# Kernel tuning notes

Hardware: AMD Instinct MI355X
Metric: run time of the kernel (lower is better)

The kernel has to match this reference:

```python
import jax, jax.numpy as jnp
import numpy as np
from jax import lax
from jax.scipy.special import digamma, logsumexp

EPS = 1e-9
T, K, D = 20000, 64, 32
Kp1 = K + 1


def setup_inputs():
    key = jax.random.key(0)
    ks = jax.random.split(key, 8)
    z_mu = jax.random.normal(ks[0], (T, D), dtype=jnp.float32)
    z_var = jax.random.uniform(ks[1], (T, D), minval=0.05, maxval=1.0, dtype=jnp.float32)
    mu_hat = jax.random.normal(ks[2], (Kp1, D), dtype=jnp.float32)
    kappa_hat = 0.01 + 100.0 * jax.random.uniform(ks[3], (Kp1,), dtype=jnp.float32)
    # nu_hat must exceed D+1; emulate nu0 + Nk with nu0 = max(32, D+2) = 34
    nu_hat = 34.0 + 100.0 * jax.random.uniform(ks[4], (Kp1,), dtype=jnp.float32)
    A = 0.1 * jax.random.normal(ks[5], (Kp1, D, D), dtype=jnp.float32)
    Psi_hat = jnp.eye(D, dtype=jnp.float32)[None] + jnp.einsum('kij,klj->kil', A, A)  # SPD
    phi_hat = 0.1 + 5.0 * jax.random.uniform(ks[6], (K, Kp1), dtype=jnp.float32)
    w = jax.random.uniform(ks[7], (Kp1,), minval=0.1, maxval=1.0, dtype=jnp.float32)
    pi_star = w / w.sum()
    return dict(z_mu=z_mu, z_var=z_var, mu_hat=mu_hat, kappa_hat=kappa_hat,
                nu_hat=nu_hat, Psi_hat=Psi_hat, phi_hat=phi_hat, pi_star=pi_star)


def reference(z_mu, z_var, mu_hat, kappa_hat, nu_hat, Psi_hat, phi_hat, pi_star):
    LOG2PI = float(np.log(2.0 * np.pi))
    LOG2 = float(np.log(2.0))
    # ---- expected emission log-likelihood E_q[log N(z_t | mu_k, Sigma_k)] : (T, K+1) ----
    d_arange = jnp.arange(1, D + 1, dtype=jnp.float32)
    E_logdet = (digamma((nu_hat[:, None] + 1.0 - d_arange) * 0.5).sum(-1)
                - D * LOG2 - jnp.linalg.slogdet(Psi_hat)[1])  # (Kp1,)
    Lam = nu_hat[:, None, None] * jnp.linalg.inv(Psi_hat)      # E[Lambda_k] (Kp1,D,D)
    t1 = jnp.einsum('kd,td->tk', jnp.diagonal(Lam, axis1=-2, axis2=-1), z_var)
    diff = z_mu[:, None, :] - mu_hat[None, :, :]               # (T,Kp1,D)
    t2 = jnp.einsum('tki,kij,tkj->tk', diff, Lam, diff)
    t3 = D * nu_hat / (kappa_hat * jnp.clip(nu_hat - D - 1.0, 1.0))
    log_B = -0.5 * (E_logdet[None, :] + t1 + t2 + t3[None, :] + D * LOG2PI)

    # ---- expected log transition matrix / initial dist ----
    log_A = digamma(phi_hat) - digamma(phi_hat.sum(-1, keepdims=True))  # (K,Kp1)
    log_pi = jnp.log(pi_star + EPS)                                      # (Kp1,)

    # ---- forward recursion (lax.scan over T) ----
    def fwd_step(prev, logb):
        msg = logsumexp(prev[:K, None] + log_A, axis=0)
        msg = jnp.logaddexp(msg, prev[-1] + log_pi)
        new = logb + msg
        return new, new
    a0 = log_pi + log_B[0]
    _, alphas = lax.scan(fwd_step, a0, log_B[1:])
    log_alpha = jnp.concatenate([a0[None], alphas], axis=0)  # (T,Kp1)

    # ---- backward recursion (reverse scan) ----
    def bwd_step(nxt, logb_next):
        tmp = logb_next + nxt  # (Kp1,)
        bk = logsumexp(log_A + tmp[None, :], axis=1)  # (K,)
        blast = logsumexp(log_pi + tmp)
        new = jnp.concatenate([bk, blast[None]])
        return new, new
    bT = jnp.zeros((Kp1,), dtype=log_B.dtype)
    _, betas = lax.scan(bwd_step, bT, log_B[1:], reverse=True)
    log_beta = jnp.concatenate([betas, bT[None]], axis=0)  # (T,Kp1)

    logZ = logsumexp(log_alpha[-1])
    gamma = jax.nn.softmax(log_alpha + log_beta - logZ, axis=-1)

    # ---- pairwise posteriors xi : (T-1, K, Kp1), vectorized over t ----
    bb = log_B[1:] + log_beta[1:]  # (T-1,Kp1)
    temp = jnp.logaddexp(log_alpha[:-1, :K, None] + log_A[None] + bb[:, None, :],
                         (log_pi + bb)[:, None, :])
    norm = logsumexp(temp.reshape(T - 1, K * Kp1), axis=-1)
    xi = jnp.exp(temp - norm[:, None, None])
    return gamma, xi, logZ
```

## Files before the change

kernel.cpp:

```cpp
#include <hip/hip_runtime.h>
#include <math.h>

#define T_LEN 20000
#define KST 64
#define KP1 65
#define DD 32
#define CHK 250
#define LCH 80

static __device__ __forceinline__ float wsum64(float v){
  v += __shfl_xor(v, 1);  v += __shfl_xor(v, 2);  v += __shfl_xor(v, 4);
  v += __shfl_xor(v, 8);  v += __shfl_xor(v, 16); v += __shfl_xor(v, 32);
  return v;
}
static __device__ __forceinline__ float wmax64(float v){
  v = fmaxf(v, __shfl_xor(v, 1));  v = fmaxf(v, __shfl_xor(v, 2));  v = fmaxf(v, __shfl_xor(v, 4));
  v = fmaxf(v, __shfl_xor(v, 8));  v = fmaxf(v, __shfl_xor(v, 16)); v = fmaxf(v, __shfl_xor(v, 32));
  return v;
}
static __device__ __forceinline__ float readlane_f(float v, int i){
  return __int_as_float(__builtin_amdgcn_readlane(__float_as_int(v), i));
}
static __device__ __forceinline__ float digamma_f(float x){
  float r = 0.f;
  while (x < 6.f){ r -= 1.f / x; x += 1.f; }
  float xi = 1.f / x;
  float xi2 = xi * xi;
  return r + logf(x) - 0.5f * xi
       - xi2 * (0.08333333333f - xi2 * (0.008333333333f - xi2 * 0.003968253968f));
}
static __device__ __forceinline__ float rcp_nr(float s){
  float r = __builtin_amdgcn_rcpf(s);
  return r * (2.0f - s * r);
}

__global__ void prep_k(const float* __restrict__ mu, const float* __restrict__ kappa,
                       const float* __restrict__ nu, const float* __restrict__ Psi,
                       float* __restrict__ Lam, float* __restrict__ dLam,
                       float* __restrict__ constk){
  const int k = blockIdx.x, tid = threadIdx.x;
  __shared__ float P[DD][DD + 1];
  const float* Pk = Psi + k * DD * DD;
  for (int e = tid; e < DD * DD; e += 64) P[e / DD][e % DD] = Pk[e];
  __syncthreads();
  for (int c = 0; c < DD; ++c){
    if (tid == c){
      float s = P[c][c];
      for (int m = 0; m < c; ++m) s -= P[c][m] * P[c][m];
      P[c][c] = sqrtf(s);
    }
    __syncthreads();
    if (tid > c && tid < DD){
      float s = P[tid][c];
      for (int m = 0; m < c; ++m) s -= P[tid][m] * P[c][m];
      P[tid][c] = s / P[c][c];
    }
    __syncthreads();
  }
  const float nuk = nu[k];
  if (tid < DD){
    float y[DD];
    #pragma unroll
    for (int r2 = 0; r2 < DD; ++r2){
      float s = (r2 == tid) ? 1.f : 0.f;
      #pragma unroll
      for (int m = 0; m < r2; ++m) s -= P[r2][m] * y[m];
      y[r2] = s / P[r2][r2];
    }
    #pragma unroll
    for (int r2 = DD - 1; r2 >= 0; --r2){
      float s = y[r2];
      #pragma unroll
      for (int m = r2 + 1; m < DD; ++m) s -= P[m][r2] * y[m];
      y[r2] = s / P[r2][r2];
    }
    #pragma unroll
    for (int i = 0; i < DD; ++i) Lam[k * DD * DD + i * DD + tid] = nuk * y[i];
    dLam[k * DD + tid] = nuk * y[tid];
  }
  float dg = 0.f, ld = 0.f;
  if (tid < DD){
    dg = digamma_f((nuk + 1.f - (float)(tid + 1)) * 0.5f);
    ld = logf(P[tid][tid]);
  }
  dg = wsum64(dg);
  ld = wsum64(ld);
  if (tid == 0){
    const float LOG2 = 0.6931471805599453f, LOG2PI = 1.8378770664093453f;
    float logdet = 2.f * ld;
    float Elogdet = dg - DD * LOG2 - logdet;
    float t3 = DD * nuk / (kappa[k] * fmaxf(nuk - DD - 1.f, 1.f));
    constk[k] = -0.5f * (Elogdet + t3 + DD * LOG2PI);
  }
}

__global__ void prep_trans(const float* __restrict__ phi, const float* __restrict__ pi_star,
                           float* __restrict__ M_mat, float* __restrict__ MT,
                           float* __restrict__ logA, float* __restrict__ logpi){
  const int i = threadIdx.x;
  float rs = 0.f;
  for (int j = 0; j < KP1; ++j) rs += phi[i * KP1 + j];
  float dgs = digamma_f(rs);
  for (int j = 0; j < KP1; ++j){
    float la = digamma_f(phi[i * KP1 + j]) - dgs;
    logA[i * KP1 + j] = la;
    float e = expf(la);
    M_mat[i * 68 + j] = e;
    MT[j * 68 + i] = e;
  }
  if (i == 0){
    for (int j = 0; j < KP1; ++j){
      float pe = pi_star[j] + 1e-9f;
      logpi[j] = logf(pe);
      M_mat[64 * 68 + j] = pe;
      MT[j * 68 + 64] = pe;
    }
  }
}

__global__ void logb_k(const float* __restrict__ zmu, const float* __restrict__ zvar,
                       const float* __restrict__ mu, const float* __restrict__ Lam,
                       const float* __restrict__ dLam, const float* __restrict__ constk,
                       float* __restrict__ logB){
  const int k = blockIdx.y, tid = threadIdx.x;
  const int t = blockIdx.x * 256 + tid;
  __shared__ float Ls[DD * DD];
  __shared__ float mus[DD], dls[DD];
  for (int e = tid; e < DD * DD; e += 256) Ls[e] = Lam[k * DD * DD + e];
  if (tid < DD){ mus[tid] = mu[k * DD + tid]; dls[tid] = dLam[k * DD + tid]; }
  __syncthreads();
  if (t >= T_LEN) return;
  const float4* zm4 = reinterpret_cast<const float4*>(zmu + (size_t)t * DD);
  const float4* zv4 = reinterpret_cast<const float4*>(zvar + (size_t)t * DD);
  float d[DD];
  float acc1 = 0.f;
  #pragma unroll
  for (int q = 0; q < DD / 4; ++q){
    float4 vm = zm4[q]; float4 vv = zv4[q];
    d[4*q+0] = vm.x - mus[4*q+0];
    d[4*q+1] = vm.y - mus[4*q+1];
    d[4*q+2] = vm.z - mus[4*q+2];
    d[4*q+3] = vm.w - mus[4*q+3];
    acc1 = fmaf(dls[4*q+0], vv.x, acc1);
    acc1 = fmaf(dls[4*q+1], vv.y, acc1);
    acc1 = fmaf(dls[4*q+2], vv.z, acc1);
    acc1 = fmaf(dls[4*q+3], vv.w, acc1);
  }
  float acc2 = 0.f;
  #pragma unroll
  for (int i = 0; i < DD; ++i){
    float s = 0.f;
    #pragma unroll
    for (int q = 0; q < DD/4; ++q){
      float4 L4 = *reinterpret_cast<const float4*>(&Ls[i*DD + q*4]);
      s = fmaf(L4.x, d[q*4+0], s);
      s = fmaf(L4.y, d[q*4+1], s);
      s = fmaf(L4.z, d[q*4+2], s);
      s = fmaf(L4.w, d[q*4+3], s);
    }
    acc2 = fmaf(s, d[i], acc2);
  }
  logB[(size_t)t * KP1 + k] = constk[k] - 0.5f * (acc1 + acc2);
}

__global__ void bexp_k(const float* __restrict__ logB, float* __restrict__ Bexp,
                       float* __restrict__ bmax){
  const int lane = threadIdx.x & 63, w = threadIdx.x >> 6;
  const int t = blockIdx.x * 4 + w;
  if (t >= T_LEN) return;
  float v = logB[(size_t)t * KP1 + lane];
  float v64 = logB[(size_t)t * KP1 + 64];
  float m = fmaxf(wmax64(v), v64);
  Bexp[(size_t)t * KP1 + lane] = expf(v - m);
  if (lane == 0){ Bexp[(size_t)t * KP1 + 64] = expf(v64 - m); bmax[t] = m; }
}

__global__ __launch_bounds__(64) void p1_k(const float* __restrict__ MT_g,
    const float* __restrict__ Bexp, float* __restrict__ S){
  __shared__ float MTl[65 * 68];
  __shared__ float Xl[64 * 65];
  const int lane = threadIdx.x;
  const int dir = blockIdx.y;
  for (int e = lane; e < 65 * 68; e += 64) MTl[e] = MT_g[e];
  __syncthreads();
  const int bx = blockIdx.x;
  const bool service = bx >= CHK;
  const int c = service ? bx - CHK : bx;
  int r0, r1;
  if (dir == 0){ r0 = 1 + c * LCH; r1 = min((c + 1) * LCH, T_LEN - 1); }
  else {
    int ue = min((c + 1) * LCH, T_LEN - 1) - 1;
    r0 = (T_LEN - 1) - ue; r1 = (T_LEN - 1) - c * LCH;
  }
  float* Sc = S + (size_t)(dir * CHK + c) * 4290;
  float* sig_out = Sc + 4225;

  if (!service){
    #pragma unroll
    for (int k = 0; k < 65; ++k) Xl[lane * 65 + k] = (k == lane) ? 1.f : 0.f;
    float rs = 1.f, sig = 0.f;
    float bvec = Bexp[(size_t)r0 * KP1 + lane];
    float b64  = Bexp[(size_t)r0 * KP1 + 64];
    for (int r = r0; r <= r1; ++r){
      float bvn = 0.f, b64n = 0.f;
      if (r < r1){
        bvn  = Bexp[(size_t)(r + 1) * KP1 + lane];
        b64n = Bexp[(size_t)(r + 1) * KP1 + 64];
      }
      float Xr[65];
      #pragma unroll
      for (int k = 0; k < 65; ++k) Xr[k] = Xl[lane * 65 + k] * rs;
      #pragma unroll
      for (int k = 0; k < 65; ++k) Xl[lane * 65 + k] = 0.f;
      unsigned long long mask = __ballot(bvec != 0.f);
      float cmax = 0.f;
      while (mask){
        int i = __builtin_ctzll(mask); mask &= mask - 1;
        float bi = readlane_f(bvec, i);
        const float* Mr = &MTl[i * 68];
        float a0 = 0.f, a1 = 0.f, a2 = 0.f, a3 = 0.f;
        #pragma unroll
        for (int g = 0; g < 16; ++g){
          float4 m4 = *reinterpret_cast<const float4*>(&Mr[g * 4]);
          a0 = fmaf(m4.x, Xr[g * 4 + 0], a0);
          a1 = fmaf(m4.y, Xr[g * 4 + 1], a1);
          a2 = fmaf(m4.z, Xr[g * 4 + 2], a2);
          a3 = fmaf(m4.w, Xr[g * 4 + 3], a3);
        }
        float sum = ((a0 + a1) + (a2 + a3)) + Mr[64] * Xr[64];
        float nv = bi * sum;
        Xl[lane * 65 + i] = nv;
        cmax = fmaxf(cmax, nv);
      }
      if (b64 != 0.f){
        const float* Mr = &MTl[64 * 68];
        float a0 = 0.f, a1 = 0.f, a2 = 0.f, a3 = 0.f;
        #pragma unroll
        for (int g = 0; g < 16; ++g){
          float4 m4 = *reinterpret_cast<const float4*>(&Mr[g * 4]);
          a0 = fmaf(m4.x, Xr[g * 4 + 0], a0);
          a1 = fmaf(m4.y, Xr[g * 4 + 1], a1);
          a2 = fmaf(m4.z, Xr[g * 4 + 2], a2);
          a3 = fmaf(m4.w, Xr[g * 4 + 3], a3);
        }
        float sum = ((a0 + a1) + (a2 + a3)) + Mr[64] * Xr[64];
        float nv = b64 * sum;
        Xl[lane * 65 + 64] = nv;
        cmax = fmaxf(cmax, nv);
      }
      float s = wmax64(cmax);
      s = fmaxf(s, 1e-37f);
      sig += logf(s);
      rs = 1.f / s;
      bvec = bvn; b64 = b64n;
    }
    for (int k = 0; k < 65; ++k) Sc[k * 65 + lane] = Xl[lane * 65 + k] * rs;
    sig_out[lane] = sig;
  } else {
    float v = 0.f, v64 = 1.f, sig = 0.f;
    float bvec = Bexp[(size_t)r0 * KP1 + lane];
    float b64  = Bexp[(size_t)r0 * KP1 + 64];
    for (int r = r0; r <= r1; ++r){
      float bvn = 0.f, b64n = 0.f;
      if (r < r1){
        bvn  = Bexp[(size_t)(r + 1) * KP1 + lane];
        b64n = Bexp[(size_t)(r + 1) * KP1 + 64];
      }
      unsigned long long mask = __ballot(bvec != 0.f);
      float vn = 0.f, v64n = 0.f;
      while (mask){
        int i = __builtin_ctzll(mask); mask &= mask - 1;
        float mi = MTl[i * 68 + lane];
        float t = mi * v;
        float sum = wsum64(t) + MTl[i * 68 + 64] * v64;
        float bi = readlane_f(bvec, i);
        vn = (lane == i) ? bi * sum : vn;
      }
      if (b64 != 0.f){
        float t = MTl[64 * 68 + lane] * v;
        float sum = wsum64(t) + MTl[64 * 68 + 64] * v64;
        v64n = b64 * sum;
      }
      float m = wmax64(vn);
      m = fmaxf(m, v64n);
      m = fmaxf(m, 1e-37f);
      float irs = 1.f / m;
      v = vn * irs; v64 = v64n * irs;
      sig += logf(m);
      bvec = bvn; b64 = b64n;
    }
    Sc[lane * 65 + 64] = v;
    if (lane == 0){ Sc[64 * 65 + 64] = v64; sig_out[64] = sig; }
  }
}

__global__ __launch_bounds__(256) void p2_k(const float* __restrict__ S,
    const float* __restrict__ M_mat, const float* __restrict__ Bexp,
    float* __restrict__ vstore){
  const int dir = blockIdx.x, tid = threadIdx.x;
  __shared__ float Sl[4290];
  __shared__ float vl[66];
  __shared__ float red[1];
  if (dir == 0){
    if (tid < 65) vl[tid] = M_mat[64 * 68 + tid] * Bexp[tid];
  } else {
    if (tid < 65) vl[tid] = 1.f;
  }
  __syncthreads();
  if (tid < 64){
    float x = vl[tid];
    float s = wsum64(x) + vl[64];
    if (tid == 0) red[0] = 1.f / s;
  }
  __syncthreads();
  if (tid < 65) vl[tid] *= red[0];
  const float* Sg = S + (size_t)dir * CHK * 4290;
  float sb[17];
  #pragma unroll
  for (int u = 0; u < 17; ++u){
    int e = tid + 256 * u;
    sb[u] = (e < 4290) ? Sg[e] : 0.f;
  }
  for (int c = 0; c < CHK; ++c){
    __syncthreads();
    #pragma unroll
    for (int u = 0; u < 17; ++u){
      int e = tid + 256 * u;
      if (e < 4290) Sl[e] = sb[u];
    }
    __syncthreads();
    if (c + 1 < CHK){
      const float* Sn = Sg + (size_t)(c + 1) * 4290;
      #pragma unroll
      for (int u = 0; u < 17; ++u){
        int e = tid + 256 * u;
        sb[u] = (e < 4290) ? Sn[e] : 0.f;
      }
    }
    if (tid < 65){
      vstore[(size_t)(dir * CHK + c) * KP1 + tid] = vl[tid];
      float sm = fmaxf(Sl[4225], Sl[4225 + 64]);
      vl[tid] = vl[tid] * expf(Sl[4225 + tid] - sm);
    }
    __syncthreads();
    float vn = 0.f;
    if (tid < 65){
      if (dir == 0){
        for (int j = 0; j < 65; ++j) vn = fmaf(Sl[tid * 65 + j], vl[j], vn);
      } else {
        for (int k = 0; k < 65; ++k) vn = fmaf(Sl[k * 65 + tid], vl[k], vn);
      }
    }
    __syncthreads();
    if (tid < 65) vl[tid] = vn;
    __syncthreads();
    if (tid < 64){
      float x = vl[tid];
      float s = wsum64(x) + vl[64];
      if (tid == 0) red[0] = 1.f / fmaxf(s, 1e-37f);
    }
    __syncthreads();
    if (tid < 65) vl[tid] *= red[0];
  }
}

__global__ __launch_bounds__(64) void p3_k(const float* __restrict__ M_mat,
    const float* __restrict__ MT_g, const float* __restrict__ Bexp,
    const float* __restrict__ bmax, const float* __restrict__ vstore,
    float* __restrict__ pstore, float* __restrict__ qstore,
    float* __restrict__ cfor, float* __restrict__ csum){
  __shared__ float Ml[65 * 68];
  const int lane = threadIdx.x;
  const int c = blockIdx.x, dir = blockIdx.y;
  const float* src = (dir == 0) ? M_mat : MT_g;
  for (int e = lane; e < 65 * 68; e += 64) Ml[e] = src[e];
  __syncthreads();
  if (dir == 0){
    float p, p64, sig;
    const int r0 = 1 + c * LCH, r1 = min((c + 1) * LCH, T_LEN - 1);
    if (c == 0){
      float pe = Ml[64 * 68 + lane], pe64 = Ml[64 * 68 + 64];
      float b = Bexp[lane], b64v = Bexp[64];
      float val = pe * b, v64 = pe64 * b64v;
      float s = wsum64(val) + v64;
      float rr = 1.f / s;
      p = val * rr; p64 = v64 * rr;
      pstore[lane] = p; if (lane == 0) pstore[64] = p64;
      sig = logf(s) + bmax[0];
      if (lane == 0) cfor[0] = sig;
    } else {
      p = vstore[(size_t)c * KP1 + lane];
      p64 = vstore[(size_t)c * KP1 + 64];
      sig = 0.f;
    }
    float bvec = Bexp[(size_t)r0 * KP1 + lane], b64 = Bexp[(size_t)r0 * KP1 + 64];
    for (int r = r0; r <= r1; ++r){
      float bvn = 0.f, b64n = 0.f;
      if (r < r1){
        bvn = Bexp[(size_t)(r + 1) * KP1 + lane]; b64n = Bexp[(size_t)(r + 1) * KP1 + 64];
      }
      unsigned long long mask = __ballot(p != 0.f);
      float msg = 0.f, msg64 = 0.f;
      while (mask){
        int i = __builtin_ctzll(mask); mask &= mask - 1;
        float pi_ = readlane_f(p, i);
        msg   = fmaf(pi_, Ml[i * 68 + lane], msg);
        msg64 = fmaf(pi_, Ml[i * 68 + 64], msg64);
      }
      if (p64 != 0.f){
        msg   = fmaf(p64, Ml[64 * 68 + lane], msg);
        msg64 = fmaf(p64, Ml[64 * 68 + 64], msg64);
      }
      float val = bvec * msg, v64 = b64 * msg64;
      float s = wsum64(val) + v64;
      float rr = 1.f / s;
      p = val * rr; p64 = v64 * rr;
      pstore[(size_t)r * KP1 + lane] = p;
      if (lane == 0) pstore[(size_t)r * KP1 + 64] = p64;
      sig += logf(s) + bmax[r];
      if (lane == 0) cfor[r] = sig;
      bvec = bvn; b64 = b64n;
    }
    if (lane == 0) csum[c] = sig;
  } else {
    float q, q64;
    const int ustart = c * LCH;
    const int ue = min((c + 1) * LCH, T_LEN - 1) - 1;
    if (c == 0){
      q = 1.f / 65.f; q64 = 1.f / 65.f;
      qstore[(size_t)(T_LEN - 1) * KP1 + lane] = q;
      if (lane == 0) qstore[(size_t)(T_LEN - 1) * KP1 + 64] = q64;
    } else {
      q = vstore[(size_t)(CHK + c) * KP1 + lane];
      q64 = vstore[(size_t)(CHK + c) * KP1 + 64];
    }
    int rfirst = (T_LEN - 1) - ustart;
    float bvec = Bexp[(size_t)rfirst * KP1 + lane], b64 = Bexp[(size_t)rfirst * KP1 + 64];
    for (int u = ustart; u <= ue; ++u){
      int r = (T_LEN - 1) - u;
      float bvn = 0.f, b64n = 0.f;
      if (u < ue){
        bvn = Bexp[(size_t)(r - 1) * KP1 + lane]; b64n = Bexp[(size_t)(r - 1) * KP1 + 64];
      }
      float x = bvec * q, x64 = b64 * q64;
      unsigned long long mask = __ballot(x != 0.f);
      float acc = 0.f, acc64 = 0.f;
      while (mask){
        int k = __builtin_ctzll(mask); mask &= mask - 1;
        float xk = readlane_f(x, k);
        acc   = fmaf(xk, Ml[k * 68 + lane], acc);
        acc64 = fmaf(xk, Ml[k * 68 + 64], acc64);
      }
      if (x64 != 0.f){
        acc   = fmaf(x64, Ml[64 * 68 + lane], acc);
        acc64 = fmaf(x64, Ml[64 * 68 + 64], acc64);
      }
      float s = wsum64(acc) + acc64;
      float rr = 1.f / s;
      q = acc * rr; q64 = acc64 * rr;
      qstore[(size_t)(r - 1) * KP1 + lane] = q;
      if (lane == 0) qstore[(size_t)(r - 1) * KP1 + 64] = q64;
      bvec = bvn; b64 = b64n;
    }
  }
}

__global__ __launch_bounds__(64) void pfx_k(const float* __restrict__ csum,
    float* __restrict__ coff, float* __restrict__ logZ){
  __shared__ float cs[CHK], co[CHK + 1];
  const int lane = threadIdx.x;
  for (int e = lane; e < CHK; e += 64) cs[e] = csum[e];
  __syncthreads();
  if (lane == 0){
    float a = 0.f;
    for (int c = 0; c < CHK; ++c){ co[c] = a; a += cs[c]; }
    co[CHK] = a;
    logZ[0] = a;
  }
  __syncthreads();
  for (int e = lane; e < CHK; e += 64) coff[e] = co[e];
}

__global__ void off_k(float* __restrict__ cfor, const float* __restrict__ coff){
  int t = blockIdx.x * 256 + threadIdx.x;
  if (t >= T_LEN) return;
  int c = (t == 0) ? 0 : (t - 1) / LCH;
  cfor[t] += coff[c];
}

__global__ void gamma_k(const float* __restrict__ pstore, const float* __restrict__ qstore,
                        float* __restrict__ gout){
  const int lane = threadIdx.x & 63, w = threadIdx.x >> 6;
  const int t = blockIdx.x * 4 + w;
  if (t >= T_LEN) return;
  float a   = pstore[(size_t)t * KP1 + lane] * qstore[(size_t)t * KP1 + lane];
  float a64 = pstore[(size_t)t * KP1 + 64]   * qstore[(size_t)t * KP1 + 64];
  float s = wsum64(a) + a64;
  float r = rcp_nr(s);
  gout[(size_t)t * KP1 + lane] = a * r;
  if (lane == 0) gout[(size_t)t * KP1 + 64] = a64 * r;
}

__global__ void xi_k(const float* __restrict__ pstore, const float* __restrict__ qstore,
                     const float* __restrict__ logB, const float* __restrict__ cfor,
                     const float* __restrict__ logA, const float* __restrict__ logpi,
                     float* __restrict__ xiout){
  const int t = blockIdx.x, tid = threadIdx.x;
  __shared__ float laS[64], bbS[KP1], lpiS[KP1];
  __shared__ float red[4], red2[4];
  if (tid < 64){
    laS[tid] = logf(pstore[(size_t)t * KP1 + tid]) + cfor[t];
  } else if (tid < 64 + KP1){
    int j = tid - 64;
    bbS[j] = logB[(size_t)(t + 1) * KP1 + j] + logf(qstore[(size_t)(t + 1) * KP1 + j]);
  } else if (tid < 64 + 2 * KP1){
    int j = tid - (64 + KP1);
    lpiS[j] = logpi[j];
  }
  __syncthreads();
  float tv[17];
  float lm = -3.0e38f;
  #pragma unroll
  for (int r2 = 0; r2 < 17; ++r2){
    int e = tid + 256 * r2;
    if (e < KST * KP1){
      int i = e / KP1;
      int j = e - i * KP1;
      float a = laS[i] + logA[e];
      float b = lpiS[j];
      float mx = fmaxf(a, b), mn = fminf(a, b);
      float v = bbS[j] + mx + log1pf(expf(mn - mx));
      tv[r2] = v;
      lm = fmaxf(lm, v);
    } else tv[r2] = -3.0e38f;
  }
  lm = wmax64(lm);
  if ((tid & 63) == 0) red[tid >> 6] = lm;
  __syncthreads();
  float gm = fmaxf(fmaxf(red[0], red[1]), fmaxf(red[2], red[3]));
  float se = 0.f;
  #pragma unroll
  for (int r2 = 0; r2 < 17; ++r2) se += expf(tv[r2] - gm);
  se = wsum64(se);
  if ((tid & 63) == 0) red2[tid >> 6] = se;
  __syncthreads();
  float S = red2[0] + red2[1] + red2[2] + red2[3];
  float rS = rcp_nr(S);
  float* xrow = xiout + (size_t)t * (KST * KP1);
  #pragma unroll
  for (int r2 = 0; r2 < 17; ++r2){
    int e = tid + 256 * r2;
    if (e < KST * KP1) xrow[e] = expf(tv[r2] - gm) * rS;
  }
}

extern "C" void kernel_launch(void* const* d_in, const int* in_sizes, int n_in,
                              void* d_out, int out_size, void* d_ws, size_t ws_size,
                              hipStream_t stream){
  const float* z_mu  = (const float*)d_in[0];
  const float* z_var = (const float*)d_in[1];
  const float* mu    = (const float*)d_in[2];
  const float* kappa = (const float*)d_in[3];
  const float* nu    = (const float*)d_in[4];
  const float* Psi   = (const float*)d_in[5];
  const float* phi   = (const float*)d_in[6];
  const float* pis   = (const float*)d_in[7];
  float* out = (float*)d_out;

  float* ws     = (float*)d_ws;
  float* Lam    = ws;
  float* dLam   = Lam + 66560;
  float* constk = dLam + 2080;
  float* M_mat  = constk + 65;
  float* MT     = M_mat + 4420;
  float* logA   = MT + 4420;
  float* logpi  = logA + 4160;
  float* logB   = logpi + 65;
  float* Bexp   = logB + 1300000;
  float* bmax   = Bexp + 1300000;
  float* pstore = bmax + 20000;
  float* qstore = pstore + 1300000;
  float* cfor   = qstore + 1300000;
  float* S      = cfor + 20000;
  float* vstore = S + 2145000;
  float* csum   = vstore + 32500;
  float* coff   = csum + 256;

  float* gammaOut = out;
  float* xiOut    = gammaOut + (size_t)T_LEN * KP1;
  float* logZOut  = xiOut + (size_t)(T_LEN - 1) * KST * KP1;

  prep_k<<<KP1, 64, 0, stream>>>(mu, kappa, nu, Psi, Lam, dLam, constk);
  prep_trans<<<1, 64, 0, stream>>>(phi, pis, M_mat, MT, logA, logpi);
  logb_k<<<dim3((T_LEN + 255) / 256, KP1), 256, 0, stream>>>(z_mu, z_var, mu, Lam, dLam, constk, logB);
  bexp_k<<<(T_LEN + 3) / 4, 256, 0, stream>>>(logB, Bexp, bmax);
  p1_k<<<dim3(2 * CHK, 2), 64, 0, stream>>>(MT, Bexp, S);
  p2_k<<<2, 256, 0, stream>>>(S, M_mat, Bexp, vstore);
  p3_k<<<dim3(CHK, 2), 64, 0, stream>>>(M_mat, MT, Bexp, bmax, vstore, pstore, qstore, cfor, csum);
  pfx_k<<<1, 64, 0, stream>>>(csum, coff, logZOut);
  off_k<<<(T_LEN + 255) / 256, 256, 0, stream>>>(cfor, coff);
  gamma_k<<<(T_LEN + 3) / 4, 256, 0, stream>>>(pstore, qstore, gammaOut);
  xi_k<<<T_LEN - 1, 256, 0, stream>>>(pstore, qstore, logB, cfor, logA, logpi, xiOut);
}
```

Measured before the change: 1.365 ms.

## Add hierarchical chunk-operator scan, sparse transfer products, and xi smem/logaddexp tweaks

```diff
diff --git a/kernel.cpp b/kernel.cpp
--- a/kernel.cpp
+++ b/kernel.cpp
@@ -7,6 +7,9 @@
 #define DD 32
 #define CHK 250
 #define LCH 80
+#define GSZ 10
+#define NG 25
+#define OPS 4296
 
 static __device__ __forceinline__ float wsum64(float v){
   v += __shfl_xor(v, 1);  v += __shfl_xor(v, 2);  v += __shfl_xor(v, 4);
@@ -178,7 +181,7 @@
 __global__ __launch_bounds__(64) void p1_k(const float* __restrict__ MT_g,
     const float* __restrict__ Bexp, float* __restrict__ S){
   __shared__ float MTl[65 * 68];
-  __shared__ float Xl[64 * 65];
+  __shared__ float Xbuf[2][65][64];
   const int lane = threadIdx.x;
   const int dir = blockIdx.y;
   for (int e = lane; e < 65 * 68; e += 64) MTl[e] = MT_g[e];
@@ -192,70 +195,103 @@
     int ue = min((c + 1) * LCH, T_LEN - 1) - 1;
     r0 = (T_LEN - 1) - ue; r1 = (T_LEN - 1) - c * LCH;
   }
-  float* Sc = S + (size_t)(dir * CHK + c) * 4290;
+  float* Sc = S + (size_t)(dir * CHK + c) * OPS;
   float* sig_out = Sc + 4225;
 
   if (!service){
-    #pragma unroll
-    for (int k = 0; k < 65; ++k) Xl[lane * 65 + k] = (k == lane) ? 1.f : 0.f;
     float rs = 1.f, sig = 0.f;
-    float bvec = Bexp[(size_t)r0 * KP1 + lane];
-    float b64  = Bexp[(size_t)r0 * KP1 + 64];
+    unsigned long long pmask = 0; bool pb64 = false;
+    unsigned long long dirty0 = ~0ull, dirty1 = ~0ull;
+    bool dirty64_0 = true, dirty64_1 = true;
+    int cur = 0;
+    float bv0 = Bexp[(size_t)r0 * KP1 + lane];
+    float b640 = Bexp[(size_t)r0 * KP1 + 64];
+    float bv1 = 0.f, b641 = 0.f;
+    if (r0 + 1 <= r1){ bv1 = Bexp[(size_t)(r0+1) * KP1 + lane]; b641 = Bexp[(size_t)(r0+1) * KP1 + 64]; }
     for (int r = r0; r <= r1; ++r){
-      float bvn = 0.f, b64n = 0.f;
-      if (r < r1){
-        bvn  = Bexp[(size_t)(r + 1) * KP1 + lane];
-        b64n = Bexp[(size_t)(r + 1) * KP1 + 64];
-      }
-      float Xr[65];
-      #pragma unroll
-      for (int k = 0; k < 65; ++k) Xr[k] = Xl[lane * 65 + k] * rs;
-      #pragma unroll
-      for (int k = 0; k < 65; ++k) Xl[lane * 65 + k] = 0.f;
-      unsigned long long mask = __ballot(bvec != 0.f);
+      float bv2 = 0.f, b642 = 0.f;
+      if (r + 2 <= r1){ bv2 = Bexp[(size_t)(r+2) * KP1 + lane]; b642 = Bexp[(size_t)(r+2) * KP1 + 64]; }
+      unsigned long long nmask = __ballot(bv0 != 0.f);
+      bool nb64 = (b640 != 0.f);
+      const int nb = cur ^ 1;
       float cmax = 0.f;
-      while (mask){
-        int i = __builtin_ctzll(mask); mask &= mask - 1;
-        float bi = readlane_f(bvec, i);
-        const float* Mr = &MTl[i * 68];
-        float a0 = 0.f, a1 = 0.f, a2 = 0.f, a3 = 0.f;
-        #pragma unroll
-        for (int g = 0; g < 16; ++g){
-          float4 m4 = *reinterpret_cast<const float4*>(&Mr[g * 4]);
-          a0 = fmaf(m4.x, Xr[g * 4 + 0], a0);
-          a1 = fmaf(m4.y, Xr[g * 4 + 1], a1);
-          a2 = fmaf(m4.z, Xr[g * 4 + 2], a2);
-          a3 = fmaf(m4.w, Xr[g * 4 + 3], a3);
+      if (r == r0){
+        unsigned long long m = nmask;
+        while (m){
+          int i = __builtin_ctzll(m); m &= m - 1;
+          float nv = readlane_f(bv0, i) * MTl[i*68 + lane];
+          Xbuf[nb][i][lane] = nv; cmax = fmaxf(cmax, nv);
         }
-        float sum = ((a0 + a1) + (a2 + a3)) + Mr[64] * Xr[64];
-        float nv = bi * sum;
-        Xl[lane * 65 + i] = nv;
-        cmax = fmaxf(cmax, nv);
-      }
-      if (b64 != 0.f){
-        const float* Mr = &MTl[64 * 68];
-        float a0 = 0.f, a1 = 0.f, a2 = 0.f, a3 = 0.f;
-        #pragma unroll
-        for (int g = 0; g < 16; ++g){
-          float4 m4 = *reinterpret_cast<const float4*>(&Mr[g * 4]);
-          a0 = fmaf(m4.x, Xr[g * 4 + 0], a0);
-          a1 = fmaf(m4.y, Xr[g * 4 + 1], a1);
-          a2 = fmaf(m4.z, Xr[g * 4 + 2], a2);
-          a3 = fmaf(m4.w, Xr[g * 4 + 3], a3);
+        if (nb64){
+          float nv = b640 * MTl[64*68 + lane];
+          Xbuf[nb][64][lane] = nv; cmax = fmaxf(cmax, nv);
         }
-        float sum = ((a0 + a1) + (a2 + a3)) + Mr[64] * Xr[64];
-        float nv = b64 * sum;
-        Xl[lane * 65 + 64] = nv;
-        cmax = fmaxf(cmax, nv);
-      }
-      float s = wmax64(cmax);
-      s = fmaxf(s, 1e-37f);
+      } else {
+        const bool dense = __builtin_popcountll(pmask) >= 24;
+        for (int pass = 0; pass < 2; ++pass){
+          if (pass == 1 && !nb64) break;
+          unsigned long long mm = (pass == 0) ? nmask : 1ull;
+          while (mm){
+            int i;
+            if (pass == 0){ i = __builtin_ctzll(mm); mm &= mm - 1; }
+            else { i = 64; mm = 0; }
+            float acc = 0.f;
+            if (dense){
+              #pragma unroll
+              for (int g4 = 0; g4 < 16; ++g4){
+                float4 m4 = *reinterpret_cast<const float4*>(&MTl[i*68 + 4*g4]);
+                acc = fmaf(m4.x, Xbuf[cur][4*g4+0][lane], acc);
+                acc = fmaf(m4.y, Xbuf[cur][4*g4+1][lane], acc);
+                acc = fmaf(m4.z, Xbuf[cur][4*g4+2][lane], acc);
+                acc = fmaf(m4.w, Xbuf[cur][4*g4+3][lane], acc);
+              }
+              acc = fmaf(MTl[i*68 + 64], Xbuf[cur][64][lane], acc);
+            } else {
+              unsigned long long jm = pmask;
+              while (jm){
+                int j = __builtin_ctzll(jm); jm &= jm - 1;
+                acc = fmaf(MTl[i*68 + j], Xbuf[cur][j][lane], acc);
+              }
+              if (pb64) acc = fmaf(MTl[i*68 + 64], Xbuf[cur][64][lane], acc);
+            }
+            float bi = (i == 64) ? b640 : readlane_f(bv0, i);
+            float nv = bi * acc * rs;
+            Xbuf[nb][i][lane] = nv;
+            cmax = fmaxf(cmax, nv);
+          }
+        }
+      }
+      {
+        unsigned long long dN = (nb == 0) ? dirty0 : dirty1;
+        bool d64N = (nb == 0) ? dirty64_0 : dirty64_1;
+        unsigned long long zm = dN & ~nmask;
+        while (zm){
+          int z = __builtin_ctzll(zm); zm &= zm - 1;
+          Xbuf[nb][z][lane] = 0.f;
+        }
+        if (d64N && !nb64) Xbuf[nb][64][lane] = 0.f;
+        if (nb == 0){ dirty0 = nmask; dirty64_0 = nb64; }
+        else        { dirty1 = nmask; dirty64_1 = nb64; }
+      }
+      float s = fmaxf(wmax64(cmax), 1e-37f);
       sig += logf(s);
       rs = 1.f / s;
-      bvec = bvn; b64 = b64n;
-    }
-    for (int k = 0; k < 65; ++k) Sc[k * 65 + lane] = Xl[lane * 65 + k] * rs;
+      pmask = nmask; pb64 = nb64;
+      cur = nb;
+      bv0 = bv1; b640 = b641; bv1 = bv2; b641 = b642;
+    }
+    for (int i = 0; i < 65; ++i){
+      bool act = (i < 64) ? ((pmask >> i) & 1ull) : pb64;
+      float v = act ? Xbuf[cur][i][lane] * rs : 0.f;
+      Sc[i * 65 + lane] = v;
+    }
     sig_out[lane] = sig;
+    if (lane == 0){
+      unsigned int* mw = (unsigned int*)Sc;
+      mw[4290] = (unsigned int)(pmask & 0xffffffffull);
+      mw[4291] = (unsigned int)(pmask >> 32);
+      mw[4292] = pb64 ? 1u : 0u;
+    }
   } else {
     float v = 0.f, v64 = 1.f, sig = 0.f;
     float bvec = Bexp[(size_t)r0 * KP1 + lane];
@@ -294,61 +330,210 @@
   }
 }
 
-__global__ __launch_bounds__(256) void p2_k(const float* __restrict__ S,
+__global__ __launch_bounds__(256) void p2a_k(const float* __restrict__ S,
+    float* __restrict__ Gop){
+  const int tid = threadIdx.x, lane = tid & 63, wv = tid >> 6;
+  const int g = blockIdx.x, dir = blockIdx.y;
+  __shared__ float Ys[65 * 65];
+  __shared__ float Gt[65 * 65];
+  __shared__ float Scl[OPS];
+  __shared__ float ysig[65];
+  __shared__ unsigned int msh[3];
+  const float* base = S + (size_t)(dir * CHK + g * GSZ) * OPS;
+  if (dir == 0){
+    for (int e = tid; e < 4225; e += 256) Ys[e] = base[e];
+  } else {
+    for (int e = tid; e < 4225; e += 256){
+      int i = e / 65, j = e - i * 65;
+      Ys[j * 65 + i] = base[e];
+    }
+  }
+  if (tid < 65) ysig[tid] = base[4225 + tid];
+  if (tid < 3) msh[tid] = ((const unsigned int*)base)[4290 + tid];
+  __syncthreads();
+  for (int cc = 1; cc < GSZ; ++cc){
+    const float* opc = base + (size_t)cc * OPS;
+    for (int e = tid; e < OPS; e += 256) Scl[e] = opc[e];
+    __syncthreads();
+    if (wv == 0){
+      float sigm = Scl[4225 + 0];
+      float sigs = Scl[4225 + 64];
+      float smc = fmaxf(sigm, sigs);
+      float rfm = expf(sigm - smc), rfs = expf(sigs - smc);
+      if (dir == 0){
+        unsigned long long pm = (unsigned long long)msh[0] | ((unsigned long long)msh[1] << 32);
+        bool pb64 = (msh[2] & 1u) != 0;
+        const unsigned int* smw = (const unsigned int*)Scl;
+        unsigned long long im = (unsigned long long)smw[4290] | ((unsigned long long)smw[4291] << 32);
+        bool ib64 = (smw[4292] & 1u) != 0;
+        const bool dense = __builtin_popcountll(pm) >= 24;
+        float colmax = 0.f, col64max = 0.f;
+        for (int i = 0; i < 65; ++i){
+          bool act = (i < 64) ? ((im >> i) & 1ull) : ib64;
+          float acc = 0.f, acc64 = 0.f;
+          if (act){
+            if (dense){
+              for (int k = 0; k < 64; ++k)
+                acc = fmaf(Scl[i*65 + k], Ys[k*65 + lane], acc);
+              acc *= rfm;
+            } else {
+              unsigned long long jm = pm;
+              while (jm){
+                int k = __builtin_ctzll(jm); jm &= jm - 1;
+                acc = fmaf(Scl[i*65 + k], Ys[k*65 + lane], acc);
+              }
+              acc *= rfm;
+            }
+            if (pb64) acc = fmaf(rfs * Scl[i*65 + 64], Ys[64*65 + lane], acc);
+            float part = rfm * Scl[i*65 + lane] * Ys[lane*65 + 64];
+            acc64 = wsum64(part);
+            if (pb64) acc64 += rfs * Scl[i*65 + 64] * Ys[64*65 + 64];
+          }
+          Gt[i*65 + lane] = acc;
+          if (lane == 0) Gt[i*65 + 64] = acc64;
+          colmax = fmaxf(colmax, acc);
+          col64max = fmaxf(col64max, acc64);
+        }
+        float mj = fmaxf(colmax, 1e-37f);
+        float inv = 1.f / mj;
+        for (int i = 0; i < 65; ++i) Ys[i*65 + lane] = Gt[i*65 + lane] * inv;
+        ysig[lane] += logf(mj) + smc;
+        if (lane == 0){
+          float m64 = fmaxf(col64max, 1e-37f);
+          float i64 = 1.f / m64;
+          for (int i = 0; i < 65; ++i) Ys[i*65 + 64] = Gt[i*65 + 64] * i64;
+          ysig[64] += logf(m64) + smc;
+          msh[0] = (unsigned int)(im & 0xffffffffull);
+          msh[1] = (unsigned int)(im >> 32);
+          msh[2] = ib64 ? 1u : 0u;
+        }
+      } else {
+        float colmax = 0.f, col64max = 0.f;
+        for (int i = 0; i < 65; ++i){
+          float acc = 0.f;
+          for (int k = 0; k < 64; ++k)
+            acc = fmaf(Scl[k*65 + i], Ys[k*65 + lane], acc);
+          acc *= rfm;
+          acc = fmaf(rfs * Scl[64*65 + i], Ys[64*65 + lane], acc);
+          float part = rfm * Scl[lane*65 + i] * Ys[lane*65 + 64];
+          float acc64 = wsum64(part) + rfs * Scl[64*65 + i] * Ys[64*65 + 64];
+          Gt[i*65 + lane] = acc;
+          if (lane == 0) Gt[i*65 + 64] = acc64;
+          colmax = fmaxf(colmax, acc);
+          col64max = fmaxf(col64max, acc64);
+        }
+        float mj = fmaxf(colmax, 1e-37f);
+        float inv = 1.f / mj;
+        for (int i = 0; i < 65; ++i) Ys[i*65 + lane] = Gt[i*65 + lane] * inv;
+        ysig[lane] += logf(mj) + smc;
+        if (lane == 0){
+          float m64 = fmaxf(col64max, 1e-37f);
+          float i64 = 1.f / m64;
+          for (int i = 0; i < 65; ++i) Ys[i*65 + 64] = Gt[i*65 + 64] * i64;
+          ysig[64] += logf(m64) + smc;
+        }
+      }
+    }
+    __syncthreads();
+  }
+  float* outp = Gop + (size_t)(dir * NG + g) * OPS;
+  for (int e = tid; e < 4225; e += 256) outp[e] = Ys[e];
+  if (tid < 65) outp[4225 + tid] = ysig[tid];
+  if (tid < 3) ((unsigned int*)outp)[4290 + tid] = msh[tid];
+}
+
+__global__ __launch_bounds__(256) void p2b_k(const float* __restrict__ Gop,
     const float* __restrict__ M_mat, const float* __restrict__ Bexp,
-    float* __restrict__ vstore){
+    float* __restrict__ gseed){
   const int dir = blockIdx.x, tid = threadIdx.x;
-  __shared__ float Sl[4290];
+  __shared__ float Sl[OPS];
   __shared__ float vl[66];
-  __shared__ float red[1];
-  if (dir == 0){
-    if (tid < 65) vl[tid] = M_mat[64 * 68 + tid] * Bexp[tid];
-  } else {
-    if (tid < 65) vl[tid] = 1.f;
-  }
+  __shared__ float red[2];
+  if (dir == 0){ if (tid < 65) vl[tid] = M_mat[64*68 + tid] * Bexp[tid]; }
+  else { if (tid < 65) vl[tid] = 1.f; }
   __syncthreads();
   if (tid < 64){
     float x = vl[tid];
     float s = wsum64(x) + vl[64];
-    if (tid == 0) red[0] = 1.f / s;
+    if (tid == 0) red[0] = 1.f / fmaxf(s, 1e-37f);
   }
   __syncthreads();
   if (tid < 65) vl[tid] *= red[0];
-  const float* Sg = S + (size_t)dir * CHK * 4290;
+  const float* Gg = Gop + (size_t)dir * NG * OPS;
   float sb[17];
   #pragma unroll
-  for (int u = 0; u < 17; ++u){
-    int e = tid + 256 * u;
-    sb[u] = (e < 4290) ? Sg[e] : 0.f;
-  }
-  for (int c = 0; c < CHK; ++c){
+  for (int u = 0; u < 17; ++u){ int e = tid + 256*u; sb[u] = (e < OPS) ? Gg[e] : 0.f; }
+  for (int c = 0; c < NG; ++c){
     __syncthreads();
     #pragma unroll
-    for (int u = 0; u < 17; ++u){
-      int e = tid + 256 * u;
-      if (e < 4290) Sl[e] = sb[u];
-    }
-    __syncthreads();
-    if (c + 1 < CHK){
-      const float* Sn = Sg + (size_t)(c + 1) * 4290;
+    for (int u = 0; u < 17; ++u){ int e = tid + 256*u; if (e < OPS) Sl[e] = sb[u]; }
+    __syncthreads();
+    if (c + 1 < NG){
+      const float* Sn = Gg + (size_t)(c+1) * OPS;
       #pragma unroll
-      for (int u = 0; u < 17; ++u){
-        int e = tid + 256 * u;
-        sb[u] = (e < 4290) ? Sn[e] : 0.f;
-      }
-    }
+      for (int u = 0; u < 17; ++u){ int e = tid + 256*u; sb[u] = (e < OPS) ? Sn[e] : 0.f; }
+    }
+    if (tid < 65) gseed[(size_t)(dir * NG + c) * KP1 + tid] = vl[tid];
+    if (tid < 64){
+      float gm = wmax64(Sl[4225 + tid]);
+      if (tid == 0) red[1] = fmaxf(gm, Sl[4225 + 64]);
+    }
+    __syncthreads();
+    if (tid < 65) vl[tid] = vl[tid] * expf(Sl[4225 + tid] - red[1]);
+    __syncthreads();
+    float vn = 0.f;
     if (tid < 65){
-      vstore[(size_t)(dir * CHK + c) * KP1 + tid] = vl[tid];
-      float sm = fmaxf(Sl[4225], Sl[4225 + 64]);
-      vl[tid] = vl[tid] * expf(Sl[4225 + tid] - sm);
-    }
+      for (int j = 0; j < 65; ++j) vn = fmaf(Sl[tid*65 + j], vl[j], vn);
+    }
+    __syncthreads();
+    if (tid < 65) vl[tid] = vn;
+    __syncthreads();
+    if (tid < 64){
+      float x = vl[tid];
+      float s = wsum64(x) + vl[64];
+      if (tid == 0) red[0] = 1.f / fmaxf(s, 1e-37f);
+    }
+    __syncthreads();
+    if (tid < 65) vl[tid] *= red[0];
+  }
+}
+
+__global__ __launch_bounds__(256) void p2c_k(const float* __restrict__ S,
+    const float* __restrict__ gseed, float* __restrict__ vstore){
+  const int g = blockIdx.x, dir = blockIdx.y, tid = threadIdx.x;
+  __shared__ float Sl[OPS];
+  __shared__ float vl[66];
+  __shared__ float red[2];
+  if (tid < 65) vl[tid] = gseed[(size_t)(dir * NG + g) * KP1 + tid];
+  const float* base = S + (size_t)(dir * CHK + g * GSZ) * OPS;
+  float sb[17];
+  #pragma unroll
+  for (int u = 0; u < 17; ++u){ int e = tid + 256*u; sb[u] = (e < OPS) ? base[e] : 0.f; }
+  for (int cc = 0; cc < GSZ; ++cc){
+    __syncthreads();
+    #pragma unroll
+    for (int u = 0; u < 17; ++u){ int e = tid + 256*u; if (e < OPS) Sl[e] = sb[u]; }
+    __syncthreads();
+    if (cc + 1 < GSZ){
+      const float* Sn = base + (size_t)(cc+1) * OPS;
+      #pragma unroll
+      for (int u = 0; u < 17; ++u){ int e = tid + 256*u; sb[u] = (e < OPS) ? Sn[e] : 0.f; }
+    }
+    const int cid = g * GSZ + cc;
+    if (tid < 65) vstore[(size_t)(dir * CHK + cid) * KP1 + tid] = vl[tid];
+    if (tid < 64){
+      float gm = wmax64(Sl[4225 + tid]);
+      if (tid == 0) red[1] = fmaxf(gm, Sl[4225 + 64]);
+    }
+    __syncthreads();
+    if (tid < 65) vl[tid] = vl[tid] * expf(Sl[4225 + tid] - red[1]);
     __syncthreads();
     float vn = 0.f;
     if (tid < 65){
       if (dir == 0){
-        for (int j = 0; j < 65; ++j) vn = fmaf(Sl[tid * 65 + j], vl[j], vn);
+        for (int j = 0; j < 65; ++j) vn = fmaf(Sl[tid*65 + j], vl[j], vn);
       } else {
-        for (int k = 0; k < 65; ++k) vn = fmaf(Sl[k * 65 + tid], vl[k], vn);
+        for (int k = 0; k < 65; ++k) vn = fmaf(Sl[k*65 + tid], vl[k], vn);
       }
     }
     __syncthreads();
@@ -383,10 +568,10 @@
       float b = Bexp[lane], b64v = Bexp[64];
       float val = pe * b, v64 = pe64 * b64v;
       float s = wsum64(val) + v64;
-      float rr = 1.f / s;
+      float rr = 1.f / fmaxf(s, 1e-37f);
       p = val * rr; p64 = v64 * rr;
       pstore[lane] = p; if (lane == 0) pstore[64] = p64;
-      sig = logf(s) + bmax[0];
+      sig = logf(fmaxf(s, 1e-37f)) + bmax[0];
       if (lane == 0) cfor[0] = sig;
     } else {
       p = vstore[(size_t)c * KP1 + lane];
@@ -413,11 +598,11 @@
       }
       float val = bvec * msg, v64 = b64 * msg64;
       float s = wsum64(val) + v64;
-      float rr = 1.f / s;
+      float rr = 1.f / fmaxf(s, 1e-37f);
       p = val * rr; p64 = v64 * rr;
       pstore[(size_t)r * KP1 + lane] = p;
       if (lane == 0) pstore[(size_t)r * KP1 + 64] = p64;
-      sig += logf(s) + bmax[r];
+      sig += logf(fmaxf(s, 1e-37f)) + bmax[r];
       if (lane == 0) cfor[r] = sig;
       bvec = bvn; b64 = b64n;
     }
@@ -456,7 +641,7 @@
         acc64 = fmaf(x64, Ml[64 * 68 + 64], acc64);
       }
       float s = wsum64(acc) + acc64;
-      float rr = 1.f / s;
+      float rr = 1.f / fmaxf(s, 1e-37f);
       q = acc * rr; q64 = acc64 * rr;
       qstore[(size_t)(r - 1) * KP1 + lane] = q;
       if (lane == 0) qstore[(size_t)(r - 1) * KP1 + 64] = q64;
@@ -496,18 +681,21 @@
   float a   = pstore[(size_t)t * KP1 + lane] * qstore[(size_t)t * KP1 + lane];
   float a64 = pstore[(size_t)t * KP1 + 64]   * qstore[(size_t)t * KP1 + 64];
   float s = wsum64(a) + a64;
-  float r = rcp_nr(s);
+  float r = rcp_nr(fmaxf(s, 1e-37f));
   gout[(size_t)t * KP1 + lane] = a * r;
   if (lane == 0) gout[(size_t)t * KP1 + 64] = a64 * r;
 }
 
-__global__ void xi_k(const float* __restrict__ pstore, const float* __restrict__ qstore,
+__global__ __launch_bounds__(256) void xi_k(const float* __restrict__ pstore,
+                     const float* __restrict__ qstore,
                      const float* __restrict__ logB, const float* __restrict__ cfor,
-                     const float* __restrict__ logA, const float* __restrict__ logpi,
+                     const float* __restrict__ logA_g, const float* __restrict__ logpi,
                      float* __restrict__ xiout){
   const int t = blockIdx.x, tid = threadIdx.x;
   __shared__ float laS[64], bbS[KP1], lpiS[KP1];
+  __shared__ float lA[KST * KP1];
   __shared__ float red[4], red2[4];
+  for (int e = tid; e < KST * KP1; e += 256) lA[e] = logA_g[e];
   if (tid < 64){
     laS[tid] = logf(pstore[(size_t)t * KP1 + tid]) + cfor[t];
   } else if (tid < 64 + KP1){
@@ -518,39 +706,43 @@
     lpiS[j] = logpi[j];
   }
   __syncthreads();
-  float tv[17];
-  float lm = -3.0e38f;
+  float uu[17], ww[17];
+  float um = -3.0e38f;
   #pragma unroll
   for (int r2 = 0; r2 < 17; ++r2){
     int e = tid + 256 * r2;
     if (e < KST * KP1){
       int i = e / KP1;
       int j = e - i * KP1;
-      float a = laS[i] + logA[e];
+      float a = laS[i] + lA[e];
       float b = lpiS[j];
       float mx = fmaxf(a, b), mn = fminf(a, b);
-      float v = bbS[j] + mx + log1pf(expf(mn - mx));
-      tv[r2] = v;
-      lm = fmaxf(lm, v);
-    } else tv[r2] = -3.0e38f;
-  }
-  lm = wmax64(lm);
-  if ((tid & 63) == 0) red[tid >> 6] = lm;
-  __syncthreads();
-  float gm = fmaxf(fmaxf(red[0], red[1]), fmaxf(red[2], red[3]));
+      uu[r2] = bbS[j] + mx;
+      ww[r2] = 1.f + expf(mn - mx);
+      um = fmaxf(um, uu[r2]);
+    } else { uu[r2] = -3.0e38f; ww[r2] = 0.f; }
+  }
+  um = wmax64(um);
+  if ((tid & 63) == 0) red[tid >> 6] = um;
+  __syncthreads();
+  float R = fmaxf(fmaxf(red[0], red[1]), fmaxf(red[2], red[3]));
   float se = 0.f;
   #pragma unroll
-  for (int r2 = 0; r2 < 17; ++r2) se += expf(tv[r2] - gm);
+  for (int r2 = 0; r2 < 17; ++r2){
+    float e_ = ww[r2] * expf(uu[r2] - R);
+    uu[r2] = e_;
+    se += e_;
+  }
   se = wsum64(se);
   if ((tid & 63) == 0) red2[tid >> 6] = se;
   __syncthreads();
-  float S = red2[0] + red2[1] + red2[2] + red2[3];
-  float rS = rcp_nr(S);
+  float Ssum = red2[0] + red2[1] + red2[2] + red2[3];
+  float rS = rcp_nr(Ssum);
   float* xrow = xiout + (size_t)t * (KST * KP1);
   #pragma unroll
   for (int r2 = 0; r2 < 17; ++r2){
     int e = tid + 256 * r2;
-    if (e < KST * KP1) xrow[e] = expf(tv[r2] - gm) * rS;
+    if (e < KST * KP1) xrow[e] = uu[r2] * rS;
   }
 }
 
@@ -582,7 +774,9 @@
   float* qstore = pstore + 1300000;
   float* cfor   = qstore + 1300000;
   float* S      = cfor + 20000;
-  float* vstore = S + 2145000;
+  float* Gop    = S + 2148000;
+  float* gseed  = Gop + 214800;
+  float* vstore = gseed + 3250;
   float* csum   = vstore + 32500;
   float* coff   = csum + 256;
 
@@ -595,7 +789,9 @@
   logb_k<<<dim3((T_LEN + 255) / 256, KP1), 256, 0, stream>>>(z_mu, z_var, mu, Lam, dLam, constk, logB);
   bexp_k<<<(T_LEN + 3) / 4, 256, 0, stream>>>(logB, Bexp, bmax);
   p1_k<<<dim3(2 * CHK, 2), 64, 0, stream>>>(MT, Bexp, S);
-  p2_k<<<2, 256, 0, stream>>>(S, M_mat, Bexp, vstore);
+  p2a_k<<<dim3(NG, 2), 256, 0, stream>>>(S, Gop);
+  p2b_k<<<2, 256, 0, stream>>>(Gop, M_mat, Bexp, gseed);
+  p2c_k<<<dim3(NG, 2), 256, 0, stream>>>(S, gseed, vstore);
   p3_k<<<dim3(CHK, 2), 64, 0, stream>>>(M_mat, MT, Bexp, bmax, vstore, pstore, qstore, cfor, csum);
   pfx_k<<<1, 64, 0, stream>>>(csum, coff, logZOut);
   off_k<<<(T_LEN + 255) / 256, 256, 0, stream>>>(cfor, coff);
```

New measurement: 1.767 ms. 29.4% more time.
